# Performance work log

Measured on AMD Instinct MI355X. Metric: run time of the kernel, lower is better.

Reference implementation:

```python
import jax, jax.numpy as jnp
import numpy as np
from jax import lax

WIN_SIZE = 11
WIN_SIGMA = 1.5
DATA_RANGE = 1.0
K1, K2 = 0.01, 0.03


def _gauss_1d(win_size, sigma):
    coords = jnp.arange(win_size, dtype=jnp.float32) - win_size // 2
    g = jnp.exp(-(coords ** 2) / (2.0 * sigma ** 2))
    return g / jnp.sum(g)


def _gauss_filter(x, win):
    # Separable depthwise gaussian blur, VALID padding (matches pytorch_msssim).
    C = x.shape[1]
    kh = jnp.tile(win.reshape(1, 1, -1, 1), (C, 1, 1, 1))  # (C,1,k,1)
    kw = jnp.tile(win.reshape(1, 1, 1, -1), (C, 1, 1, 1))  # (C,1,1,k)
    dn = ('NCHW', 'OIHW', 'NCHW')
    x = lax.conv_general_dilated(x, kh, (1, 1), 'VALID',
                                 dimension_numbers=dn, feature_group_count=C)
    x = lax.conv_general_dilated(x, kw, (1, 1), 'VALID',
                                 dimension_numbers=dn, feature_group_count=C)
    return x


def _ssim(X, Y, win, data_range):
    C1 = (K1 * data_range) ** 2
    C2 = (K2 * data_range) ** 2
    mu1 = _gauss_filter(X, win)
    mu2 = _gauss_filter(Y, win)
    mu1_sq = mu1 * mu1
    mu2_sq = mu2 * mu2
    mu1_mu2 = mu1 * mu2
    sigma1_sq = _gauss_filter(X * X, win) - mu1_sq
    sigma2_sq = _gauss_filter(Y * Y, win) - mu2_sq
    sigma12 = _gauss_filter(X * Y, win) - mu1_mu2
    cs_map = (2.0 * sigma12 + C2) / (sigma1_sq + sigma2_sq + C2)
    ssim_map = ((2.0 * mu1_mu2 + C1) / (mu1_sq + mu2_sq + C1)) * cs_map
    return jnp.mean(ssim_map)


def setup_inputs() -> dict:
    key = jax.random.key(0)
    k1, k2 = jax.random.split(key)
    shape = (16, 3, 384, 512)
    pred = jax.random.uniform(k1, shape, dtype=jnp.float32)
    target = jax.random.uniform(k2, shape, dtype=jnp.float32)
    return {"pred": pred, "target": target}


def reference(pred, target):
    win = _gauss_1d(WIN_SIZE, WIN_SIGMA)
    ssim_val = _ssim(pred, target, win, DATA_RANGE)
    return 1.0 - ssim_val
```

## Files before the change

### kernel.cpp

```cpp
#include <hip/hip_runtime.h>
#include <math.h>

#define WIN 11
#define IMG_H 384
#define IMG_W 512
#define OUT_H (IMG_H - WIN + 1)
#define OUT_W (IMG_W - WIN + 1)
#define ROWS_PER_BLOCK 4
#define NBLK_X ((OUT_H + ROWS_PER_BLOCK - 1) / ROWS_PER_BLOCK)
#define NBUCKETS 256

struct GaussW { float g[WIN]; };

#define HORIZ_CH(acc, out)                                                  \
    {                                                                       \
        float v[18];                                                        \
        _Pragma("unroll")                                                   \
        for (int j = 0; j < 8; ++j) v[j] = acc[j];                          \
        _Pragma("unroll")                                                   \
        for (int j = 0; j < 8; ++j) v[8 + j] = __shfl(acc[j], lane + 1, 64);\
        v[16] = __shfl(acc[0], lane + 2, 64);                               \
        v[17] = __shfl(acc[1], lane + 2, 64);                               \
        _Pragma("unroll")                                                   \
        for (int j = 0; j < 8; ++j) {                                       \
            float o = 0.f;                                                  \
            _Pragma("unroll")                                               \
            for (int k = 0; k < WIN; ++k) o = fmaf(gw.g[k], v[j + k], o);   \
            out[j] = o;                                                     \
        }                                                                   \
    }

__global__ __launch_bounds__(64 * ROWS_PER_BLOCK) void ssim_fused_kernel(
    const float* __restrict__ X, const float* __restrict__ Y,
    double* __restrict__ accum, GaussW gw)
{
    const int wave = threadIdx.x >> 6;
    const int lane = threadIdx.x & 63;
    const int row  = blockIdx.x * ROWS_PER_BLOCK + wave;
    const int img  = blockIdx.y;
    if (row >= OUT_H) return;

    const int c0 = lane << 3;
    const float* __restrict__ px = X + ((size_t)img * IMG_H + row) * IMG_W + c0;
    const float* __restrict__ py = Y + ((size_t)img * IMG_H + row) * IMG_W + c0;

    float m1[8], m2[8], xx[8], yy[8], xy[8];
    #pragma unroll
    for (int j = 0; j < 8; ++j) { m1[j] = m2[j] = xx[j] = yy[j] = xy[j] = 0.f; }

    #pragma unroll
    for (int k = 0; k < WIN; ++k) {
        float4 xa = *(const float4*)(px + k * IMG_W);
        float4 xb = *(const float4*)(px + k * IMG_W + 4);
        float4 ya = *(const float4*)(py + k * IMG_W);
        float4 yb = *(const float4*)(py + k * IMG_W + 4);
        float xs[8] = {xa.x, xa.y, xa.z, xa.w, xb.x, xb.y, xb.z, xb.w};
        float ys[8] = {ya.x, ya.y, ya.z, ya.w, yb.x, yb.y, yb.z, yb.w};
        const float g = gw.g[k];
        #pragma unroll
        for (int j = 0; j < 8; ++j) {
            float x = xs[j], y = ys[j];
            m1[j] = fmaf(g, x, m1[j]);
            m2[j] = fmaf(g, y, m2[j]);
            float t = g * x;
            xx[j] = fmaf(t, x, xx[j]);
            xy[j] = fmaf(t, y, xy[j]);
            float u = g * y;
            yy[j] = fmaf(u, y, yy[j]);
        }
    }

    float h1[8], h2[8], hxx[8], hyy[8], hxy[8];
    HORIZ_CH(m1, h1)
    HORIZ_CH(m2, h2)
    HORIZ_CH(xx, hxx)
    HORIZ_CH(yy, hyy)
    HORIZ_CH(xy, hxy)

    const float C1 = 1e-4f, C2 = 9e-4f;
    float sum = 0.f;
    #pragma unroll
    for (int j = 0; j < 8; ++j) {
        float mu1 = h1[j], mu2 = h2[j];
        float mu1s = mu1 * mu1, mu2s = mu2 * mu2, m12 = mu1 * mu2;
        float s1  = hxx[j] - mu1s;
        float s2  = hyy[j] - mu2s;
        float s12 = hxy[j] - m12;
        float num = fmaf(2.f, m12, C1) * fmaf(2.f, s12, C2);
        float den = (mu1s + mu2s + C1) * (s1 + s2 + C2);
        float ssim = num * __builtin_amdgcn_rcpf(den);
        sum += (c0 + j < OUT_W) ? ssim : 0.f;
    }

    #pragma unroll
    for (int off = 32; off; off >>= 1)
        sum += __shfl_down(sum, off, 64);
    if (lane == 0) {
        int gwid = (blockIdx.y * NBLK_X + blockIdx.x) * ROWS_PER_BLOCK + wave;
        atomicAdd(&accum[gwid & (NBUCKETS - 1)], (double)sum);
    }
}

__global__ void ssim_finalize_kernel(const double* __restrict__ accum,
                                     float* __restrict__ out, double inv_count)
{
    const int lane = threadIdx.x;
    double s = 0.0;
    for (int i = lane; i < NBUCKETS; i += 64) s += accum[i];
    #pragma unroll
    for (int off = 32; off; off >>= 1)
        s += __shfl_down(s, off, 64);
    if (lane == 0) out[0] = (float)(1.0 - s * inv_count);
}

extern "C" void kernel_launch(void* const* d_in, const int* in_sizes, int n_in,
                              void* d_out, int out_size, void* d_ws, size_t ws_size,
                              hipStream_t stream) {
    const float* X = (const float*)d_in[0];
    const float* Y = (const float*)d_in[1];
    float* out = (float*)d_out;
    double* accum = (double*)d_ws;

    const int NC = 16 * 3;

    GaussW gw;
    {
        double g[WIN], ssum = 0.0;
        for (int i = 0; i < WIN; ++i) {
            double d = (double)i - WIN / 2;
            g[i] = exp(-(d * d) / (2.0 * 1.5 * 1.5));
            ssum += g[i];
        }
        for (int i = 0; i < WIN; ++i) gw.g[i] = (float)(g[i] / ssum);
    }

    hipMemsetAsync(accum, 0, NBUCKETS * sizeof(double), stream);

    dim3 grid(NBLK_X, NC);
    ssim_fused_kernel<<<grid, 64 * ROWS_PER_BLOCK, 0, stream>>>(X, Y, accum, gw);

    const double inv_count = 1.0 / ((double)NC * OUT_H * OUT_W);
    ssim_finalize_kernel<<<1, 64, 0, stream>>>(accum, out, inv_count);
}
```

Measured before the change: 149.3 us.

## Compute two output rows per wave and remap blocks across XCDs

Each wave now produces two adjacent output rows from 12 loaded input rows instead of one row from 11, so each loaded row feeds two vertical accumulations and per-output global loads drop. Blocks are launched as a 1D grid and remapped so that consecutive bands of the same image land on the same XCD, which should improve L2 reuse of the overlapping input rows. The cost is double the accumulator registers, which may lower occupancy. Out-of-range rows are clamped on load and masked on output.

```diff
diff --git a/kernel.cpp b/kernel.cpp
--- a/kernel.cpp
+++ b/kernel.cpp
@@ -6,97 +6,125 @@
 #define IMG_W 512
 #define OUT_H (IMG_H - WIN + 1)
 #define OUT_W (IMG_W - WIN + 1)
-#define ROWS_PER_BLOCK 4
-#define NBLK_X ((OUT_H + ROWS_PER_BLOCK - 1) / ROWS_PER_BLOCK)
+#define RPW 2
+#define WAVES_PER_BLOCK 4
+#define ROWS_PER_BLOCK (RPW * WAVES_PER_BLOCK)
+#define BANDS_PER_IMG ((OUT_H + ROWS_PER_BLOCK - 1) / ROWS_PER_BLOCK)
+#define NIMG 48
+#define NBLOCKS (BANDS_PER_IMG * NIMG)
+#define BLOCKS_PER_XCD (NBLOCKS / 8)
 #define NBUCKETS 256
 
 struct GaussW { float g[WIN]; };
 
-#define HORIZ_CH(acc, out)                                                  \
-    {                                                                       \
-        float v[18];                                                        \
-        _Pragma("unroll")                                                   \
-        for (int j = 0; j < 8; ++j) v[j] = acc[j];                          \
-        _Pragma("unroll")                                                   \
-        for (int j = 0; j < 8; ++j) v[8 + j] = __shfl(acc[j], lane + 1, 64);\
-        v[16] = __shfl(acc[0], lane + 2, 64);                               \
-        v[17] = __shfl(acc[1], lane + 2, 64);                               \
-        _Pragma("unroll")                                                   \
-        for (int j = 0; j < 8; ++j) {                                       \
-            float o = 0.f;                                                  \
-            _Pragma("unroll")                                               \
-            for (int k = 0; k < WIN; ++k) o = fmaf(gw.g[k], v[j + k], o);   \
-            out[j] = o;                                                     \
-        }                                                                   \
+__device__ __forceinline__ void horiz11(const float (&acc)[8], float (&out)[8],
+                                        int lane, const GaussW& gw)
+{
+    float v[18];
+    #pragma unroll
+    for (int j = 0; j < 8; ++j) v[j] = acc[j];
+    #pragma unroll
+    for (int j = 0; j < 8; ++j) v[8 + j] = __shfl(acc[j], lane + 1, 64);
+    v[16] = __shfl(acc[0], lane + 2, 64);
+    v[17] = __shfl(acc[1], lane + 2, 64);
+    #pragma unroll
+    for (int j = 0; j < 8; ++j) {
+        float o = 0.f;
+        #pragma unroll
+        for (int k = 0; k < WIN; ++k) o = fmaf(gw.g[k], v[j + k], o);
+        out[j] = o;
     }
+}
 
-__global__ __launch_bounds__(64 * ROWS_PER_BLOCK) void ssim_fused_kernel(
+__device__ __forceinline__ float row_ssim(float (&acc)[5][8], int lane, int c0,
+                                          const GaussW& gw)
+{
+    float h[5][8];
+    #pragma unroll
+    for (int ch = 0; ch < 5; ++ch) horiz11(acc[ch], h[ch], lane, gw);
+    const float C1 = 1e-4f, C2 = 9e-4f;
+    float s = 0.f;
+    #pragma unroll
+    for (int j = 0; j < 8; ++j) {
+        float mu1 = h[0][j], mu2 = h[1][j];
+        float mu1s = mu1 * mu1, mu2s = mu2 * mu2, m12 = mu1 * mu2;
+        float s1  = h[2][j] - mu1s;
+        float s2  = h[3][j] - mu2s;
+        float s12 = h[4][j] - m12;
+        float num = fmaf(2.f, m12, C1) * fmaf(2.f, s12, C2);
+        float den = (mu1s + mu2s + C1) * (s1 + s2 + C2);
+        float ssim = num * __builtin_amdgcn_rcpf(den);
+        s += (c0 + j < OUT_W) ? ssim : 0.f;
+    }
+    return s;
+}
+
+__global__ __launch_bounds__(64 * WAVES_PER_BLOCK) void ssim_fused_kernel(
     const float* __restrict__ X, const float* __restrict__ Y,
     double* __restrict__ accum, GaussW gw)
 {
     const int wave = threadIdx.x >> 6;
     const int lane = threadIdx.x & 63;
-    const int row  = blockIdx.x * ROWS_PER_BLOCK + wave;
-    const int img  = blockIdx.y;
-    if (row >= OUT_H) return;
+
+    const int id   = blockIdx.x;
+    const int wid  = (id & 7) * BLOCKS_PER_XCD + (id >> 3);
+    const int img  = wid / BANDS_PER_IMG;
+    const int band = wid % BANDS_PER_IMG;
+    const int r0   = band * ROWS_PER_BLOCK + wave * RPW;
 
     const int c0 = lane << 3;
-    const float* __restrict__ px = X + ((size_t)img * IMG_H + row) * IMG_W + c0;
-    const float* __restrict__ py = Y + ((size_t)img * IMG_H + row) * IMG_W + c0;
+    const float* __restrict__ Xb = X + ((size_t)img * IMG_H) * IMG_W + c0;
+    const float* __restrict__ Yb = Y + ((size_t)img * IMG_H) * IMG_W + c0;
 
-    float m1[8], m2[8], xx[8], yy[8], xy[8];
+    float a[RPW][5][8];
     #pragma unroll
-    for (int j = 0; j < 8; ++j) { m1[j] = m2[j] = xx[j] = yy[j] = xy[j] = 0.f; }
+    for (int r = 0; r < RPW; ++r)
+        #pragma unroll
+        for (int ch = 0; ch < 5; ++ch)
+            #pragma unroll
+            for (int j = 0; j < 8; ++j) a[r][ch][j] = 0.f;
 
     #pragma unroll
-    for (int k = 0; k < WIN; ++k) {
-        float4 xa = *(const float4*)(px + k * IMG_W);
-        float4 xb = *(const float4*)(px + k * IMG_W + 4);
-        float4 ya = *(const float4*)(py + k * IMG_W);
-        float4 yb = *(const float4*)(py + k * IMG_W + 4);
+    for (int k = 0; k < RPW + WIN - 1; ++k) {
+        int gr = r0 + k; gr = gr < IMG_H - 1 ? gr : IMG_H - 1;
+        const float* rx = Xb + (size_t)gr * IMG_W;
+        const float* ry = Yb + (size_t)gr * IMG_W;
+        float4 xa = *(const float4*)(rx);
+        float4 xb = *(const float4*)(rx + 4);
+        float4 ya = *(const float4*)(ry);
+        float4 yb = *(const float4*)(ry + 4);
         float xs[8] = {xa.x, xa.y, xa.z, xa.w, xb.x, xb.y, xb.z, xb.w};
         float ys[8] = {ya.x, ya.y, ya.z, ya.w, yb.x, yb.y, yb.z, yb.w};
-        const float g = gw.g[k];
         #pragma unroll
-        for (int j = 0; j < 8; ++j) {
-            float x = xs[j], y = ys[j];
-            m1[j] = fmaf(g, x, m1[j]);
-            m2[j] = fmaf(g, y, m2[j]);
-            float t = g * x;
-            xx[j] = fmaf(t, x, xx[j]);
-            xy[j] = fmaf(t, y, xy[j]);
-            float u = g * y;
-            yy[j] = fmaf(u, y, yy[j]);
+        for (int r = 0; r < RPW; ++r) {
+            if (k - r >= 0 && k - r < WIN) {
+                const float g = gw.g[k - r];
+                #pragma unroll
+                for (int j = 0; j < 8; ++j) {
+                    float x = xs[j], y = ys[j];
+                    a[r][0][j] = fmaf(g, x, a[r][0][j]);
+                    a[r][1][j] = fmaf(g, y, a[r][1][j]);
+                    float t = g * x;
+                    a[r][2][j] = fmaf(t, x, a[r][2][j]);
+                    a[r][4][j] = fmaf(t, y, a[r][4][j]);
+                    float u = g * y;
+                    a[r][3][j] = fmaf(u, y, a[r][3][j]);
+                }
+            }
         }
     }
 
-    float h1[8], h2[8], hxx[8], hyy[8], hxy[8];
-    HORIZ_CH(m1, h1)
-    HORIZ_CH(m2, h2)
-    HORIZ_CH(xx, hxx)
-    HORIZ_CH(yy, hyy)
-    HORIZ_CH(xy, hxy)
-
-    const float C1 = 1e-4f, C2 = 9e-4f;
     float sum = 0.f;
     #pragma unroll
-    for (int j = 0; j < 8; ++j) {
-        float mu1 = h1[j], mu2 = h2[j];
-        float mu1s = mu1 * mu1, mu2s = mu2 * mu2, m12 = mu1 * mu2;
-        float s1  = hxx[j] - mu1s;
-        float s2  = hyy[j] - mu2s;
-        float s12 = hxy[j] - m12;
-        float num = fmaf(2.f, m12, C1) * fmaf(2.f, s12, C2);
-        float den = (mu1s + mu2s + C1) * (s1 + s2 + C2);
-        float ssim = num * __builtin_amdgcn_rcpf(den);
-        sum += (c0 + j < OUT_W) ? ssim : 0.f;
-    }
+    for (int r = 0; r < RPW; ++r)
+        if (r0 + r < OUT_H)
+            sum += row_ssim(a[r], lane, c0, gw);
 
     #pragma unroll
     for (int off = 32; off; off >>= 1)
         sum += __shfl_down(sum, off, 64);
     if (lane == 0) {
-        int gwid = (blockIdx.y * NBLK_X + blockIdx.x) * ROWS_PER_BLOCK + wave;
+        int gwid = id * WAVES_PER_BLOCK + wave;
         atomicAdd(&accum[gwid & (NBUCKETS - 1)], (double)sum);
     }
 }
@@ -121,8 +149,6 @@
     float* out = (float*)d_out;
     double* accum = (double*)d_ws;
 
-    const int NC = 16 * 3;
-
     GaussW gw;
     {
         double g[WIN], ssum = 0.0;
@@ -136,9 +162,8 @@
 
     hipMemsetAsync(accum, 0, NBUCKETS * sizeof(double), stream);
 
-    dim3 grid(NBLK_X, NC);
-    ssim_fused_kernel<<<grid, 64 * ROWS_PER_BLOCK, 0, stream>>>(X, Y, accum, gw);
+    ssim_fused_kernel<<<NBLOCKS, 64 * WAVES_PER_BLOCK, 0, stream>>>(X, Y, accum, gw);
 
-    const double inv_count = 1.0 / ((double)NC * OUT_H * OUT_W);
+    const double inv_count = 1.0 / ((double)(NIMG) * OUT_H * OUT_W);
     ssim_finalize_kernel<<<1, 64, 0, stream>>>(accum, out, inv_count);
 }
```

New measurement: 152.5 us. 1.02x slower.
